# Performance work log

Measured on AMD Instinct MI355X. Metric: run time of the kernel, lower is better.

## Reference

```python
import jax, jax.numpy as jnp
import numpy as np

N = 50000    # nodes
E = 800000   # edges (avg degree 16)
IN = 256     # in_dim
HID = 256    # hidden_dim
OUT = 128    # out_dim


def setup_inputs() -> dict:
    key = jax.random.key(0)
    ks = jax.random.split(key, 9)
    features = jax.random.normal(ks[0], (N, IN), jnp.float32)
    src = jax.random.randint(ks[1], (E,), 0, N, jnp.int32)
    dst = jax.random.randint(ks[2], (E,), 0, N, jnp.int32)
    noise = jax.random.normal(ks[3], (N, OUT), jnp.float32)
    def glorot(k, shape, fan):
        return jax.random.normal(k, shape, jnp.float32) / np.float32(np.sqrt(fan))
    W1 = glorot(ks[4], (IN, HID), IN);  b1 = jnp.zeros((HID,), jnp.float32)
    W2 = glorot(ks[5], (HID, OUT), HID); b2 = jnp.zeros((OUT,), jnp.float32)
    W3 = glorot(ks[6], (HID, OUT), HID); b3 = jnp.zeros((OUT,), jnp.float32)
    fcW = glorot(ks[7], (HID, IN), IN)   # nn.Linear(in_dim, hidden_dim).weight: [HID, IN]
    return dict(features=features, noise=noise, W1=W1, b1=b1, W2=W2, b2=b2,
                W3=W3, b3=b3, fcW=fcW, src=src, dst=dst)


def _gcn(x, W, b, src, dst, out_norm, in_norm):
    """DGL GraphConv norm='both': D_out^{-1/2} A D_in^{-1/2} X W + b."""
    x = x * out_norm[:, None]          # scale src features by out-deg^{-1/2}
    x = x @ W                          # dense transform (order commutes with SpMM)
    agg = jax.ops.segment_sum(x[src], dst, num_segments=N)  # sparse aggregate
    return agg * in_norm[:, None] + b


def reference(features, noise, W1, b1, W2, b2, W3, b3, fcW, src, dst):
    ones = jnp.ones((E,), jnp.float32)
    out_deg = jax.ops.segment_sum(ones, src, num_segments=N)
    in_deg = jax.ops.segment_sum(ones, dst, num_segments=N)
    out_norm = jnp.maximum(out_deg, 1.0) ** -0.5
    in_norm = jnp.maximum(in_deg, 1.0) ** -0.5

    h = jax.nn.relu(_gcn(features, W1, b1, src, dst, out_norm, in_norm))
    mean = jax.nn.relu(_gcn(h, W2, b2, src, dst, out_norm, in_norm))
    log_std = _gcn(h, W3, b3, src, dst, out_norm, in_norm)  # identity activation
    z = mean + noise * jnp.exp(log_std)
    seq_fts = features @ fcW.T
    return z, h, seq_fts
```

## Files before the change

### kernel.cpp

```cpp
#include <hip/hip_runtime.h>
#include <hip/hip_bf16.h>
#include <stdint.h>
#include <math.h>

#define IN_DIM 256
#define HID_DIM 256
#define OUT_DIM 128

typedef __attribute__((ext_vector_type(8))) short short8;
typedef __attribute__((ext_vector_type(4))) float floatx4;

__device__ __forceinline__ float bf2f(ushort u) {
  union { uint32_t i; float f; } v; v.i = ((uint32_t)u) << 16; return v.f;
}
__device__ __forceinline__ ushort f2bf(float f) {
  union { float f; uint32_t u; } v; v.f = f;
  uint32_t u = v.u;
  uint32_t r = u + 0x7fffu + ((u >> 16) & 1u);
  return (ushort)(r >> 16);
}

__global__ void deg_kernel(const int* __restrict__ src, const int* __restrict__ dst,
                           int* __restrict__ out_deg, int* __restrict__ in_deg, int E) {
  int e = blockIdx.x * 256 + threadIdx.x;
  if (e < E) {
    atomicAdd(&out_deg[src[e]], 1);
    atomicAdd(&in_deg[dst[e]], 1);
  }
}

__global__ void scan_sums(const int* __restrict__ deg, int* __restrict__ chunk_sum, int n) {
  __shared__ int lds[256];
  int b = blockIdx.x, t = threadIdx.x;
  int base = b * 1024 + t * 4;
  int s = 0;
  if (base + 3 < n) {
    int4 v = *(const int4*)(deg + base);
    s = v.x + v.y + v.z + v.w;
  } else {
    for (int i = 0; i < 4; ++i) if (base + i < n) s += deg[base + i];
  }
  lds[t] = s;
  __syncthreads();
  for (int off = 128; off > 0; off >>= 1) {
    if (t < off) lds[t] += lds[t + off];
    __syncthreads();
  }
  if (t == 0) chunk_sum[b] = lds[0];
}

__global__ void scan_chunks(const int* __restrict__ chunk_sum, int* __restrict__ chunk_off,
                            int nchunks, int* __restrict__ row_ptr) {
  __shared__ int lds[256];
  int t = threadIdx.x;
  int v = (t < nchunks) ? chunk_sum[t] : 0;
  lds[t] = v;
  __syncthreads();
  for (int off = 1; off < 256; off <<= 1) {
    int add = (t >= off) ? lds[t - off] : 0;
    __syncthreads();
    lds[t] += add;
    __syncthreads();
  }
  if (t < nchunks) chunk_off[t] = lds[t] - v;
  if (t == 0) row_ptr[0] = 0;
}

__global__ void scan_final(const int* __restrict__ deg, const int* __restrict__ chunk_off,
                           int* __restrict__ row_ptr, int n) {
  __shared__ int lds[256];
  int b = blockIdx.x, t = threadIdx.x;
  int base = b * 1024 + t * 4;
  int v[4]; int s = 0;
#pragma unroll
  for (int i = 0; i < 4; ++i) { v[i] = (base + i < n) ? deg[base + i] : 0; s += v[i]; }
  lds[t] = s;
  __syncthreads();
  for (int off = 1; off < 256; off <<= 1) {
    int add = (t >= off) ? lds[t - off] : 0;
    __syncthreads();
    lds[t] += add;
    __syncthreads();
  }
  int run = lds[t] - s + chunk_off[b];
#pragma unroll
  for (int i = 0; i < 4; ++i) {
    run += v[i];
    if (base + i < n) row_ptr[base + i + 1] = run;
  }
}

__global__ void fill_kernel(const int* __restrict__ src, const int* __restrict__ dst,
                            const int* __restrict__ row_ptr, int* __restrict__ fill_cnt,
                            const int* __restrict__ out_deg,
                            int2* __restrict__ edge_sw, int E) {
  int e = blockIdx.x * 256 + threadIdx.x;
  if (e < E) {
    int d = dst[e];
    int s = src[e];
    int pos = row_ptr[d] + atomicAdd(&fill_cnt[d], 1);
    int od = out_deg[s]; if (od < 1) od = 1;
    int2 rec;
    rec.x = s;
    rec.y = __float_as_int(rsqrtf((float)od));
    edge_sw[pos] = rec;
  }
}

__global__ void prep_weights(const float* __restrict__ W1, const float* __restrict__ W2,
                             const float* __restrict__ W3, const float* __restrict__ b2,
                             const float* __restrict__ b3, const float* __restrict__ fcW,
                             ushort* __restrict__ W1T, ushort* __restrict__ WcT,
                             float* __restrict__ bcat, ushort* __restrict__ fcWb) {
  int k = blockIdx.x;
  int n = threadIdx.x;
  W1T[n * 256 + k] = f2bf(W1[k * 256 + n]);
  WcT[n * 256 + k] = f2bf((n < 128) ? W2[k * 128 + n] : W3[k * 128 + (n - 128)]);
  fcWb[k * 256 + n] = f2bf(fcW[k * 256 + n]);
  if (k == 0) bcat[n] = (n < 128) ? b2[n] : b3[n - 128];
}

__global__ __launch_bounds__(256) void agg_kernel(
    const ushort* __restrict__ x, const int* __restrict__ row_ptr,
    const int2* __restrict__ edge_sw,
    const int* __restrict__ in_deg, ushort* __restrict__ out, int N) {
  int wave = threadIdx.x >> 6, lane = threadIdx.x & 63;
  int n = blockIdx.x * 4 + wave;
  if (n >= N) return;
  int half = lane >> 5;
  int hl = lane & 31;
  int start = row_ptr[n], end = row_ptr[n + 1];
  int id = in_deg[n]; if (id < 1) id = 1;
  float inn = rsqrtf((float)id);

  float acc[8];
#pragma unroll
  for (int k = 0; k < 8; ++k) acc[k] = 0.f;

  int cs[4]; float cw[4];
#pragma unroll
  for (int k = 0; k < 4; ++k) {
    int i = start + half + 2 * k;
    cs[k] = 0; cw[k] = 0.f;
    if (i < end) { int2 e = edge_sw[i]; cs[k] = e.x; cw[k] = __int_as_float(e.y); }
  }

  for (int base = start; base < end; base += 8) {
    uint4 v[4];
#pragma unroll
    for (int k = 0; k < 4; ++k)
      v[k] = *(const uint4*)&x[(size_t)cs[k] * 256 + hl * 8];

    int ns[4]; float nw[4];
#pragma unroll
    for (int k = 0; k < 4; ++k) {
      int i = base + 8 + half + 2 * k;
      ns[k] = 0; nw[k] = 0.f;
      if (i < end) { int2 e = edge_sw[i]; ns[k] = e.x; nw[k] = __int_as_float(e.y); }
    }

#pragma unroll
    for (int k = 0; k < 4; ++k) {
      const uint32_t* p = (const uint32_t*)&v[k];
      float wk = cw[k];
#pragma unroll
      for (int q = 0; q < 4; ++q) {
        acc[2 * q]     += bf2f((ushort)(p[q] & 0xffffu)) * wk;
        acc[2 * q + 1] += bf2f((ushort)(p[q] >> 16)) * wk;
      }
    }
#pragma unroll
    for (int k = 0; k < 4; ++k) { cs[k] = ns[k]; cw[k] = nw[k]; }
  }

#pragma unroll
  for (int k = 0; k < 8; ++k) acc[k] += __shfl_xor(acc[k], 32, 64);

  if (half == 0) {
    uint4 o;
    uint32_t* po = (uint32_t*)&o;
#pragma unroll
    for (int q = 0; q < 4; ++q) {
      po[q] = ((uint32_t)f2bf(acc[2 * q + 1] * inn) << 16) |
              (uint32_t)f2bf(acc[2 * q] * inn);
    }
    *(uint4*)&out[(size_t)n * 256 + hl * 8] = o;
  }
}

__global__ __launch_bounds__(256, 2) void gemm_kernel(
    const ushort* __restrict__ A, const float* __restrict__ A32,
    const ushort* __restrict__ BT,
    const float* __restrict__ bias, const float* __restrict__ noise,
    float* __restrict__ C32, ushort* __restrict__ Cbf, int M, int mode) {
  __shared__ alignas(16) ushort A_lds[128 * 72];
  __shared__ alignas(16) ushort B_lds[256 * 72];
  int t = threadIdx.x;
  int m0 = blockIdx.x * 128;
  int wave = t >> 6, lane = t & 63;
  int wm = wave * 32;
  int l15 = lane & 15, quad = lane >> 4;

  floatx4 acc[2][16];
#pragma unroll
  for (int i = 0; i < 2; ++i)
#pragma unroll
    for (int j = 0; j < 16; ++j) acc[i][j] = (floatx4)(0.f);

  for (int kc = 0; kc < 256; kc += 64) {
    if (mode == 2) {
#pragma unroll
      for (int r = 0; r < 8; ++r) {
        int idx = t + r * 256;
        int row = idx >> 4;
        int c = (idx & 15) << 2;
        int grow = m0 + row; if (grow > M - 1) grow = M - 1;
        float4 v = *(const float4*)(A32 + (size_t)grow * 256 + kc + c);
        ushort4 o;
        o.x = f2bf(v.x); o.y = f2bf(v.y); o.z = f2bf(v.z); o.w = f2bf(v.w);
        *(ushort4*)&A_lds[row * 72 + c] = o;
        *(ushort4*)(Cbf + (size_t)grow * 256 + kc + c) = o;
      }
    } else {
#pragma unroll
      for (int r = 0; r < 4; ++r) {
        int idx = t + r * 256;
        int row = idx >> 3;
        int c = (idx & 7) << 3;
        int grow = m0 + row; if (grow > M - 1) grow = M - 1;
        *(uint4*)&A_lds[row * 72 + c] = *(const uint4*)(A + (size_t)grow * 256 + kc + c);
      }
    }
#pragma unroll
    for (int r = 0; r < 8; ++r) {
      int idx = t + r * 256;
      int row = idx >> 3;
      int c = (idx & 7) << 3;
      *(uint4*)&B_lds[row * 72 + c] = *(const uint4*)(BT + (size_t)row * 256 + kc + c);
    }
    __syncthreads();
#pragma unroll
    for (int ko = 0; ko < 2; ++ko) {
      short8 a[2];
#pragma unroll
      for (int i = 0; i < 2; ++i)
        a[i] = *(const short8*)&A_lds[(wm + i * 16 + l15) * 72 + ko * 32 + quad * 8];
#pragma unroll
      for (int j = 0; j < 16; ++j) {
        short8 b = *(const short8*)&B_lds[(j * 16 + l15) * 72 + ko * 32 + quad * 8];
#pragma unroll
        for (int i = 0; i < 2; ++i)
          acc[i][j] = __builtin_amdgcn_mfma_f32_16x16x32_bf16(a[i], b, acc[i][j], 0, 0, 0);
      }
    }
    __syncthreads();
  }

  if (mode == 1) {
#pragma unroll
    for (int i = 0; i < 2; ++i) {
#pragma unroll
      for (int j = 0; j < 8; ++j) {
        int col = j * 16 + l15;
        float bm = bias[col];
        float bl = bias[col + 128];
#pragma unroll
        for (int r = 0; r < 4; ++r) {
          int row = m0 + wm + i * 16 + quad * 4 + r;
          if (row < M) {
            float mean = acc[i][j][r] + bm;
            float ls = acc[i][j + 8][r] + bl;
            size_t o = (size_t)row * 128 + col;
            C32[o] = fmaxf(mean, 0.f) + noise[o] * expf(ls);
          }
        }
      }
    }
  } else {
#pragma unroll
    for (int i = 0; i < 2; ++i) {
#pragma unroll
      for (int j = 0; j < 16; ++j) {
        int col = j * 16 + l15;
        float bv = (mode == 0) ? bias[col] : 0.f;
#pragma unroll
        for (int r = 0; r < 4; ++r) {
          int row = m0 + wm + i * 16 + quad * 4 + r;
          if (row < M) {
            float v = acc[i][j][r] + bv;
            if (mode == 0) v = fmaxf(v, 0.f);
            size_t o = (size_t)row * 256 + col;
            C32[o] = v;
            if (mode == 0) Cbf[o] = f2bf(v);
          }
        }
      }
    }
  }
}

extern "C" void kernel_launch(void* const* d_in, const int* in_sizes, int n_in,
                              void* d_out, int out_size, void* d_ws, size_t ws_size,
                              hipStream_t stream) {
  const float* features = (const float*)d_in[0];
  const float* noise    = (const float*)d_in[1];
  const float* W1 = (const float*)d_in[2];
  const float* b1 = (const float*)d_in[3];
  const float* W2 = (const float*)d_in[4];
  const float* b2 = (const float*)d_in[5];
  const float* W3 = (const float*)d_in[6];
  const float* b3 = (const float*)d_in[7];
  const float* fcW = (const float*)d_in[8];
  const int* src = (const int*)d_in[9];
  const int* dst = (const int*)d_in[10];
  const int N = in_sizes[0] / IN_DIM;
  const int E = in_sizes[9];

  float* out = (float*)d_out;
  float* z_out = out;
  float* h_out = out + (size_t)N * OUT_DIM;
  float* s_out = h_out + (size_t)N * HID_DIM;

  char* w = (char*)d_ws;
  auto carve = [&](size_t bytes) {
    char* p = w;
    w += (bytes + 255) & ~(size_t)255;
    return p;
  };
  ushort* feat_bf = (ushort*)carve((size_t)N * 256 * 2);
  ushort* h_bf    = (ushort*)carve((size_t)N * 256 * 2);
  ushort* agg_buf = (ushort*)carve((size_t)N * 256 * 2);
  ushort* W1T  = (ushort*)carve(256 * 256 * 2);
  ushort* WcT  = (ushort*)carve(256 * 256 * 2);
  ushort* fcWb = (ushort*)carve(256 * 256 * 2);
  float*  bcat = (float*)carve(256 * 4);
  int* degs    = (int*)carve((size_t)3 * N * 4);
  int* out_deg = degs;
  int* in_deg  = degs + N;
  int* fill_cnt = degs + 2 * N;
  int* row_ptr  = (int*)carve((size_t)(N + 1) * 4);
  int2* edge_sw = (int2*)carve((size_t)E * 8);
  int* chunk_sum = (int*)carve(256 * 4);
  int* chunk_off = (int*)carve(256 * 4);

  const int nchunks = (N + 1023) / 1024;

  hipMemsetAsync(degs, 0, (size_t)3 * N * 4, stream);
  deg_kernel<<<(E + 255) / 256, 256, 0, stream>>>(src, dst, out_deg, in_deg, E);
  scan_sums<<<nchunks, 256, 0, stream>>>(in_deg, chunk_sum, N);
  scan_chunks<<<1, 256, 0, stream>>>(chunk_sum, chunk_off, nchunks, row_ptr);
  scan_final<<<nchunks, 256, 0, stream>>>(in_deg, chunk_off, row_ptr, N);
  fill_kernel<<<(E + 255) / 256, 256, 0, stream>>>(src, dst, row_ptr, fill_cnt, out_deg,
                                                   edge_sw, E);

  prep_weights<<<256, 256, 0, stream>>>(W1, W2, W3, b2, b3, fcW, W1T, WcT, bcat, fcWb);

  int gblocks = (N + 127) / 128;
  gemm_kernel<<<gblocks, 256, 0, stream>>>((const ushort*)nullptr, features, fcWb,
                                           (const float*)nullptr, (const float*)nullptr,
                                           s_out, feat_bf, N, 2);
  agg_kernel<<<(N + 3) / 4, 256, 0, stream>>>(feat_bf, row_ptr, edge_sw, in_deg, agg_buf, N);
  gemm_kernel<<<gblocks, 256, 0, stream>>>(agg_buf, (const float*)nullptr, W1T, b1,
                                           (const float*)nullptr, h_out, h_bf, N, 0);
  agg_kernel<<<(N + 3) / 4, 256, 0, stream>>>(h_bf, row_ptr, edge_sw, in_deg, agg_buf, N);
  gemm_kernel<<<gblocks, 256, 0, stream>>>(agg_buf, (const float*)nullptr, WcT, bcat,
                                           noise, z_out, (ushort*)nullptr, N, 1);
}
```

Before: 537.6 us.

## Merge scan into one kernel, process two edges per thread, widen aggregation batch

Replaces the three-kernel degree prefix sum with a single 1024-thread block scan that handles 64 entries per thread. The degree and CSR fill kernels now handle two edges per thread using int2 loads. The aggregation kernel drops its software-prefetch pipeline in favour of batches of 16 edges with eight gathers in flight per half-wave, and computes in-degree from row_ptr. The aim is fewer launches and more memory-level parallelism. In exchange the scan runs on a single CU with serial per-thread work, and removing the prefetch may expose index-load latency.

```diff
diff --git a/kernel.cpp b/kernel.cpp
--- a/kernel.cpp
+++ b/kernel.cpp
@@ -22,71 +22,57 @@
 
 __global__ void deg_kernel(const int* __restrict__ src, const int* __restrict__ dst,
                            int* __restrict__ out_deg, int* __restrict__ in_deg, int E) {
-  int e = blockIdx.x * 256 + threadIdx.x;
-  if (e < E) {
+  int e = (blockIdx.x * 256 + threadIdx.x) * 2;
+  if (e + 1 < E) {
+    int2 s = *(const int2*)(src + e);
+    int2 d = *(const int2*)(dst + e);
+    atomicAdd(&out_deg[s.x], 1);
+    atomicAdd(&out_deg[s.y], 1);
+    atomicAdd(&in_deg[d.x], 1);
+    atomicAdd(&in_deg[d.y], 1);
+  } else if (e < E) {
     atomicAdd(&out_deg[src[e]], 1);
     atomicAdd(&in_deg[dst[e]], 1);
   }
 }
 
-__global__ void scan_sums(const int* __restrict__ deg, int* __restrict__ chunk_sum, int n) {
-  __shared__ int lds[256];
-  int b = blockIdx.x, t = threadIdx.x;
-  int base = b * 1024 + t * 4;
+__global__ __launch_bounds__(1024) void scan_kernel(const int* __restrict__ deg,
+                                                    int* __restrict__ row_ptr, int n) {
+  __shared__ int lds[1024];
+  int t = threadIdx.x;
+  const int CH = 64;
+  int base = t * CH;
+  int v[CH];
   int s = 0;
-  if (base + 3 < n) {
-    int4 v = *(const int4*)(deg + base);
-    s = v.x + v.y + v.z + v.w;
-  } else {
-    for (int i = 0; i < 4; ++i) if (base + i < n) s += deg[base + i];
+#pragma unroll
+  for (int j = 0; j < CH / 4; ++j) {
+    int idx = base + j * 4;
+    int4 q = make_int4(0, 0, 0, 0);
+    if (idx + 3 < n) {
+      q = *(const int4*)(deg + idx);
+    } else {
+      if (idx < n)     q.x = deg[idx];
+      if (idx + 1 < n) q.y = deg[idx + 1];
+      if (idx + 2 < n) q.z = deg[idx + 2];
+    }
+    v[j * 4 + 0] = q.x; v[j * 4 + 1] = q.y; v[j * 4 + 2] = q.z; v[j * 4 + 3] = q.w;
+    s += q.x + q.y + q.z + q.w;
   }
   lds[t] = s;
   __syncthreads();
-  for (int off = 128; off > 0; off >>= 1) {
-    if (t < off) lds[t] += lds[t + off];
-    __syncthreads();
-  }
-  if (t == 0) chunk_sum[b] = lds[0];
-}
-
-__global__ void scan_chunks(const int* __restrict__ chunk_sum, int* __restrict__ chunk_off,
-                            int nchunks, int* __restrict__ row_ptr) {
-  __shared__ int lds[256];
-  int t = threadIdx.x;
-  int v = (t < nchunks) ? chunk_sum[t] : 0;
-  lds[t] = v;
-  __syncthreads();
-  for (int off = 1; off < 256; off <<= 1) {
+  for (int off = 1; off < 1024; off <<= 1) {
     int add = (t >= off) ? lds[t - off] : 0;
     __syncthreads();
     lds[t] += add;
     __syncthreads();
   }
-  if (t < nchunks) chunk_off[t] = lds[t] - v;
+  int run = lds[t] - s;
   if (t == 0) row_ptr[0] = 0;
-}
-
-__global__ void scan_final(const int* __restrict__ deg, const int* __restrict__ chunk_off,
-                           int* __restrict__ row_ptr, int n) {
-  __shared__ int lds[256];
-  int b = blockIdx.x, t = threadIdx.x;
-  int base = b * 1024 + t * 4;
-  int v[4]; int s = 0;
-#pragma unroll
-  for (int i = 0; i < 4; ++i) { v[i] = (base + i < n) ? deg[base + i] : 0; s += v[i]; }
-  lds[t] = s;
-  __syncthreads();
-  for (int off = 1; off < 256; off <<= 1) {
-    int add = (t >= off) ? lds[t - off] : 0;
-    __syncthreads();
-    lds[t] += add;
-    __syncthreads();
-  }
-  int run = lds[t] - s + chunk_off[b];
-#pragma unroll
-  for (int i = 0; i < 4; ++i) {
-    run += v[i];
-    if (base + i < n) row_ptr[base + i + 1] = run;
+#pragma unroll
+  for (int j = 0; j < CH; ++j) {
+    int idx = base + j;
+    run += v[j];
+    if (idx < n) row_ptr[idx + 1] = run;
   }
 }
 
@@ -94,16 +80,24 @@
                             const int* __restrict__ row_ptr, int* __restrict__ fill_cnt,
                             const int* __restrict__ out_deg,
                             int2* __restrict__ edge_sw, int E) {
-  int e = blockIdx.x * 256 + threadIdx.x;
-  if (e < E) {
-    int d = dst[e];
-    int s = src[e];
+  int e = (blockIdx.x * 256 + threadIdx.x) * 2;
+  if (e + 1 < E) {
+    int2 s = *(const int2*)(src + e);
+    int2 d = *(const int2*)(dst + e);
+    int pos0 = row_ptr[d.x] + atomicAdd(&fill_cnt[d.x], 1);
+    int od0 = out_deg[s.x]; if (od0 < 1) od0 = 1;
+    int2 r0; r0.x = s.x; r0.y = __float_as_int(rsqrtf((float)od0));
+    edge_sw[pos0] = r0;
+    int pos1 = row_ptr[d.y] + atomicAdd(&fill_cnt[d.y], 1);
+    int od1 = out_deg[s.y]; if (od1 < 1) od1 = 1;
+    int2 r1; r1.x = s.y; r1.y = __float_as_int(rsqrtf((float)od1));
+    edge_sw[pos1] = r1;
+  } else if (e < E) {
+    int d = dst[e]; int s = src[e];
     int pos = row_ptr[d] + atomicAdd(&fill_cnt[d], 1);
     int od = out_deg[s]; if (od < 1) od = 1;
-    int2 rec;
-    rec.x = s;
-    rec.y = __float_as_int(rsqrtf((float)od));
-    edge_sw[pos] = rec;
+    int2 r; r.x = s; r.y = __float_as_int(rsqrtf((float)od));
+    edge_sw[pos] = r;
   }
 }
 
@@ -122,45 +116,34 @@
 
 __global__ __launch_bounds__(256) void agg_kernel(
     const ushort* __restrict__ x, const int* __restrict__ row_ptr,
-    const int2* __restrict__ edge_sw,
-    const int* __restrict__ in_deg, ushort* __restrict__ out, int N) {
+    const int2* __restrict__ edge_sw, ushort* __restrict__ out, int N) {
   int wave = threadIdx.x >> 6, lane = threadIdx.x & 63;
   int n = blockIdx.x * 4 + wave;
   if (n >= N) return;
   int half = lane >> 5;
   int hl = lane & 31;
   int start = row_ptr[n], end = row_ptr[n + 1];
-  int id = in_deg[n]; if (id < 1) id = 1;
-  float inn = rsqrtf((float)id);
+  int dg = end - start; if (dg < 1) dg = 1;
+  float inn = rsqrtf((float)dg);
 
   float acc[8];
 #pragma unroll
   for (int k = 0; k < 8; ++k) acc[k] = 0.f;
 
-  int cs[4]; float cw[4];
-#pragma unroll
-  for (int k = 0; k < 4; ++k) {
-    int i = start + half + 2 * k;
-    cs[k] = 0; cw[k] = 0.f;
-    if (i < end) { int2 e = edge_sw[i]; cs[k] = e.x; cw[k] = __int_as_float(e.y); }
-  }
-
-  for (int base = start; base < end; base += 8) {
-    uint4 v[4];
-#pragma unroll
-    for (int k = 0; k < 4; ++k)
+  for (int base = start; base < end; base += 16) {
+    int cs[8]; float cw[8];
+#pragma unroll
+    for (int k = 0; k < 8; ++k) {
+      int i = base + half + 2 * k;
+      cs[k] = 0; cw[k] = 0.f;
+      if (i < end) { int2 e = edge_sw[i]; cs[k] = e.x; cw[k] = __int_as_float(e.y); }
+    }
+    uint4 v[8];
+#pragma unroll
+    for (int k = 0; k < 8; ++k)
       v[k] = *(const uint4*)&x[(size_t)cs[k] * 256 + hl * 8];
-
-    int ns[4]; float nw[4];
-#pragma unroll
-    for (int k = 0; k < 4; ++k) {
-      int i = base + 8 + half + 2 * k;
-      ns[k] = 0; nw[k] = 0.f;
-      if (i < end) { int2 e = edge_sw[i]; ns[k] = e.x; nw[k] = __int_as_float(e.y); }
-    }
-
-#pragma unroll
-    for (int k = 0; k < 4; ++k) {
+#pragma unroll
+    for (int k = 0; k < 8; ++k) {
       const uint32_t* p = (const uint32_t*)&v[k];
       float wk = cw[k];
 #pragma unroll
@@ -169,8 +152,6 @@
         acc[2 * q + 1] += bf2f((ushort)(p[q] >> 16)) * wk;
       }
     }
-#pragma unroll
-    for (int k = 0; k < 4; ++k) { cs[k] = ns[k]; cw[k] = nw[k]; }
   }
 
 #pragma unroll
@@ -340,18 +321,13 @@
   int* fill_cnt = degs + 2 * N;
   int* row_ptr  = (int*)carve((size_t)(N + 1) * 4);
   int2* edge_sw = (int2*)carve((size_t)E * 8);
-  int* chunk_sum = (int*)carve(256 * 4);
-  int* chunk_off = (int*)carve(256 * 4);
-
-  const int nchunks = (N + 1023) / 1024;
 
   hipMemsetAsync(degs, 0, (size_t)3 * N * 4, stream);
-  deg_kernel<<<(E + 255) / 256, 256, 0, stream>>>(src, dst, out_deg, in_deg, E);
-  scan_sums<<<nchunks, 256, 0, stream>>>(in_deg, chunk_sum, N);
-  scan_chunks<<<1, 256, 0, stream>>>(chunk_sum, chunk_off, nchunks, row_ptr);
-  scan_final<<<nchunks, 256, 0, stream>>>(in_deg, chunk_off, row_ptr, N);
-  fill_kernel<<<(E + 255) / 256, 256, 0, stream>>>(src, dst, row_ptr, fill_cnt, out_deg,
-                                                   edge_sw, E);
+  int eblocks = ((E + 1) / 2 + 255) / 256;
+  deg_kernel<<<eblocks, 256, 0, stream>>>(src, dst, out_deg, in_deg, E);
+  scan_kernel<<<1, 1024, 0, stream>>>(in_deg, row_ptr, N);
+  fill_kernel<<<eblocks, 256, 0, stream>>>(src, dst, row_ptr, fill_cnt, out_deg,
+                                           edge_sw, E);
 
   prep_weights<<<256, 256, 0, stream>>>(W1, W2, W3, b2, b3, fcW, W1T, WcT, bcat, fcWb);
 
@@ -359,10 +335,10 @@
   gemm_kernel<<<gblocks, 256, 0, stream>>>((const ushort*)nullptr, features, fcWb,
                                            (const float*)nullptr, (const float*)nullptr,
                                            s_out, feat_bf, N, 2);
-  agg_kernel<<<(N + 3) / 4, 256, 0, stream>>>(feat_bf, row_ptr, edge_sw, in_deg, agg_buf, N);
+  agg_kernel<<<(N + 3) / 4, 256, 0, stream>>>(feat_bf, row_ptr, edge_sw, agg_buf, N);
   gemm_kernel<<<gblocks, 256, 0, stream>>>(agg_buf, (const float*)nullptr, W1T, b1,
                                            (const float*)nullptr, h_out, h_bf, N, 0);
-  agg_kernel<<<(N + 3) / 4, 256, 0, stream>>>(h_bf, row_ptr, edge_sw, in_deg, agg_buf, N);
+  agg_kernel<<<(N + 3) / 4, 256, 0, stream>>>(h_bf, row_ptr, edge_sw, agg_buf, N);
   gemm_kernel<<<gblocks, 256, 0, stream>>>(agg_buf, (const float*)nullptr, WcT, bcat,
                                            noise, z_out, (ushort*)nullptr, N, 1);
 }
```

New measurement: 587.7 us. +9.3%, slower.
